# Optimization experiments

Measured on AMD Instinct MI355X. Metric: run time of the kernel, lower is better.

Reference implementation:

```python
import jax, jax.numpy as jnp
import numpy as np

THRESHOLD = 0.5
ALPHA = 1.0
N, D = 100000, 256
B, K = 1024, 128


def _l2norm(x):
    # F.normalize(x, p=2, dim=-1) with eps=1e-12
    return x / jnp.maximum(jnp.linalg.norm(x, axis=-1, keepdims=True), 1e-12)


def setup_inputs() -> dict:
    key = jax.random.key(0)
    k1, k2, k3, k4, k5, k6, k7 = jax.random.split(key, 7)
    feature = jax.random.normal(k1, (N, D), dtype=jnp.float32)
    text_embedding = jax.random.normal(k2, (N, D), dtype=jnp.float32)
    virtual = jax.random.normal(k3, (1, D), dtype=jnp.float32)
    # Gumbel(0,1) noise for gumbel_softmax (tau=1), materialized for determinism
    u = jax.random.uniform(k4, (B, K, K), dtype=jnp.float32, minval=1e-6, maxval=1.0 - 1e-6)
    gumbel = -jnp.log(-jnp.log(u))
    ego_nodes = jnp.sort(jax.random.randint(k5, (B, K), 0, N, dtype=jnp.int32), axis=-1)
    edges_adj = jax.random.randint(k6, (B, K, K), 0, 2, dtype=jnp.int32)
    train_label = jax.random.randint(k7, (B,), 0, 2, dtype=jnp.int32)
    return {"feature": feature, "text_embedding": text_embedding, "virtual": virtual,
            "gumbel": gumbel, "ego_nodes": ego_nodes, "edges_adj": edges_adj,
            "train_label": train_label}


def reference(feature, text_embedding, virtual, gumbel, ego_nodes, edges_adj, train_label):
    feat = _l2norm(feature)          # self.feature (normalized in __init__)
    emb = _l2norm(text_embedding)    # self.embedding
    te_local = _l2norm(emb - virtual)            # [N, D]

    tb = te_local[ego_nodes]                     # [B, K, D] gather per ego-subgraph
    sim = jnp.einsum('bkd,bjd->bkj', tb, tb) - THRESHOLD   # [B, K, K]
    sim_sub = jax.nn.softmax(sim + gumbel, axis=-1)         # gumbel_softmax, tau=1

    adj = edges_adj.astype(sim_sub.dtype)        # scatter edges_adj[src,dst]=1, precomputed
    # s_diff: row-wise L2 norm then mean over rows
    s_diff = jnp.sqrt(jnp.sum((adj - sim_sub) ** 2, axis=-1)).mean(axis=-1)   # [B]

    emb_out = feat[ego_nodes].mean(axis=1)       # [B, D] sum(feature)/n
    emb_pg = emb[ego_nodes].mean(axis=1)         # [B, D] sum(embedding)/n  (n == K)
    f_diff = jnp.linalg.norm(emb_out - emb_pg, axis=-1)                        # [B]

    score = s_diff + ALPHA * f_diff
    score = (score - score.min()) / (score.max() - score.min())

    y = train_label.astype(score.dtype)
    eps = 1e-7  # stabilizes log at exact 0/1 (torch BCELoss clamps log at -100)
    sc = jnp.clip(score, eps, 1.0 - eps)
    bce = -(y * jnp.log(sc) + (1.0 - y) * jnp.log1p(-sc)).mean()
    loss = bce / y.shape[0]
    return score, loss
```

## Files before the change

kernel.cpp:

```cpp
#include <hip/hip_runtime.h>
#include <math.h>

#define NROWS 100000
#define DIM 256
#define BB 1024
#define KK 128
#define PITCH 264

typedef __attribute__((ext_vector_type(8))) short short8;
typedef __attribute__((ext_vector_type(4))) float float4v;

__device__ __forceinline__ unsigned short f2bf(float x) {
    unsigned u = __float_as_uint(x);
    u += 0x7FFFu + ((u >> 16) & 1u);
    return (unsigned short)(u >> 16);
}

__global__ __launch_bounds__(512) void fused_main(
    const float* __restrict__ feature,
    const float* __restrict__ text,
    const float* __restrict__ virt,
    const float* __restrict__ gumbel,
    const int*   __restrict__ ego,
    const int*   __restrict__ adj,
    float*       __restrict__ score_raw)
{
    __shared__ unsigned short tb[KK * PITCH];
    __shared__ float fpart[8][DIM];
    __shared__ float spart[8];

    const int b    = blockIdx.x;
    const int tid  = threadIdx.x;
    const int wave = tid >> 6;
    const int lane = tid & 63;

    const float4 vv = ((const float4*)virt)[lane];

    float fa0 = 0.f, fa1 = 0.f, fa2 = 0.f, fa3 = 0.f;
    const int* ego_b = ego + b * KK;

    for (int k = wave * 16; k < wave * 16 + 16; ++k) {
        const int e = ego_b[k];
        const float4 t4 = ((const float4*)(text    + (size_t)e * DIM))[lane];
        const float4 f4 = ((const float4*)(feature + (size_t)e * DIM))[lane];

        float st = t4.x*t4.x + t4.y*t4.y + t4.z*t4.z + t4.w*t4.w;
        float sf = f4.x*f4.x + f4.y*f4.y + f4.z*f4.z + f4.w*f4.w;
        #pragma unroll
        for (int m = 1; m < 64; m <<= 1) {
            st += __shfl_xor(st, m);
            sf += __shfl_xor(sf, m);
        }
        const float inv_ne = 1.f / fmaxf(sqrtf(st), 1e-12f);
        const float inv_nf = 1.f / fmaxf(sqrtf(sf), 1e-12f);

        const float ex = t4.x * inv_ne, ey = t4.y * inv_ne;
        const float ez = t4.z * inv_ne, ew = t4.w * inv_ne;
        const float wx = ex - vv.x, wy = ey - vv.y;
        const float wz = ez - vv.z, ww = ew - vv.w;
        float sw = wx*wx + wy*wy + wz*wz + ww*ww;
        #pragma unroll
        for (int m = 1; m < 64; m <<= 1) sw += __shfl_xor(sw, m);
        const float inv_nt = 1.f / fmaxf(sqrtf(sw), 1e-12f);

        fa0 += f4.x * inv_nf - ex;
        fa1 += f4.y * inv_nf - ey;
        fa2 += f4.z * inv_nf - ez;
        fa3 += f4.w * inv_nf - ew;

        ushort4 pk;
        pk.x = f2bf(wx * inv_nt);
        pk.y = f2bf(wy * inv_nt);
        pk.z = f2bf(wz * inv_nt);
        pk.w = f2bf(ww * inv_nt);
        *(ushort4*)&tb[k * PITCH + 4 * lane] = pk;
    }
    fpart[wave][4*lane + 0] = fa0;
    fpart[wave][4*lane + 1] = fa1;
    fpart[wave][4*lane + 2] = fa2;
    fpart[wave][4*lane + 3] = fa3;
    __syncthreads();

    float4v acc[8];
    const float4v zero = {0.f, 0.f, 0.f, 0.f};
    #pragma unroll
    for (int t = 0; t < 8; ++t) acc[t] = zero;

    const int g = lane >> 4;
    const int c = lane & 15;

    #pragma unroll
    for (int q = 0; q < 8; ++q) {
        const int dq = q * 32 + g * 8;
        const short8 af = *(const short8*)&tb[(wave * 16 + c) * PITCH + dq];
        short8 bf0 = *(const short8*)&tb[(0*16 + c) * PITCH + dq];
        short8 bf1 = *(const short8*)&tb[(1*16 + c) * PITCH + dq];
        short8 bf2 = *(const short8*)&tb[(2*16 + c) * PITCH + dq];
        short8 bf3 = *(const short8*)&tb[(3*16 + c) * PITCH + dq];
        short8 bf4 = *(const short8*)&tb[(4*16 + c) * PITCH + dq];
        short8 bf5 = *(const short8*)&tb[(5*16 + c) * PITCH + dq];
        short8 bf6 = *(const short8*)&tb[(6*16 + c) * PITCH + dq];
        short8 bf7 = *(const short8*)&tb[(7*16 + c) * PITCH + dq];
        acc[0] = __builtin_amdgcn_mfma_f32_16x16x32_bf16(af, bf0, acc[0], 0, 0, 0);
        acc[1] = __builtin_amdgcn_mfma_f32_16x16x32_bf16(af, bf1, acc[1], 0, 0, 0);
        acc[2] = __builtin_amdgcn_mfma_f32_16x16x32_bf16(af, bf2, acc[2], 0, 0, 0);
        acc[3] = __builtin_amdgcn_mfma_f32_16x16x32_bf16(af, bf3, acc[3], 0, 0, 0);
        acc[4] = __builtin_amdgcn_mfma_f32_16x16x32_bf16(af, bf4, acc[4], 0, 0, 0);
        acc[5] = __builtin_amdgcn_mfma_f32_16x16x32_bf16(af, bf5, acc[5], 0, 0, 0);
        acc[6] = __builtin_amdgcn_mfma_f32_16x16x32_bf16(af, bf6, acc[6], 0, 0, 0);
        acc[7] = __builtin_amdgcn_mfma_f32_16x16x32_bf16(af, bf7, acc[7], 0, 0, 0);
    }

    const float* gb = gumbel + (size_t)b * KK * KK;
    const int*   ab = adj    + (size_t)b * KK * KK;
    float rs = 0.f;
    #pragma unroll
    for (int r = 0; r < 4; ++r) {
        const int krow = wave * 16 + g * 4 + r;
        const float* gr = gb + krow * KK + c;
        const int*   ar = ab + krow * KK + c;
        float v[8];
        float mx = -1e30f;
        #pragma unroll
        for (int t = 0; t < 8; ++t) {
            v[t] = acc[t][r] - 0.5f + gr[t * 16];
            mx = fmaxf(mx, v[t]);
        }
        #pragma unroll
        for (int msk = 1; msk < 16; msk <<= 1) mx = fmaxf(mx, __shfl_xor(mx, msk));
        float S = 0.f;
        #pragma unroll
        for (int t = 0; t < 8; ++t) { v[t] = __expf(v[t] - mx); S += v[t]; }
        #pragma unroll
        for (int msk = 1; msk < 16; msk <<= 1) S += __shfl_xor(S, msk);
        const float invS = 1.f / S;
        float T = 0.f;
        #pragma unroll
        for (int t = 0; t < 8; ++t) {
            const float d = (float)ar[t * 16] - v[t] * invS;
            T += d * d;
        }
        #pragma unroll
        for (int msk = 1; msk < 16; msk <<= 1) T += __shfl_xor(T, msk);
        rs += sqrtf(T);
    }
    rs += __shfl_xor(rs, 16);
    rs += __shfl_xor(rs, 32);
    if (lane == 0) spart[wave] = rs;
    __syncthreads();

    if (wave == 0) {
        float d0 = 0.f, d1 = 0.f, d2 = 0.f, d3 = 0.f;
        #pragma unroll
        for (int w = 0; w < 8; ++w) {
            d0 += fpart[w][lane];
            d1 += fpart[w][lane + 64];
            d2 += fpart[w][lane + 128];
            d3 += fpart[w][lane + 192];
        }
        const float inv = 1.f / 128.f;
        d0 *= inv; d1 *= inv; d2 *= inv; d3 *= inv;
        float q2 = d0*d0 + d1*d1 + d2*d2 + d3*d3;
        #pragma unroll
        for (int m = 1; m < 64; m <<= 1) q2 += __shfl_xor(q2, m);
        if (lane == 0) {
            float stot = 0.f;
            #pragma unroll
            for (int w = 0; w < 8; ++w) stot += spart[w];
            score_raw[b] = stot * (1.f / 128.f) + sqrtf(q2);
        }
    }
}

__global__ __launch_bounds__(1024) void finalize(
    const float* __restrict__ score_raw,
    const int*   __restrict__ label,
    float*       __restrict__ out)
{
    __shared__ float wmin[16], wmax[16], wsum[16];
    const int tid = threadIdx.x;
    const float s = score_raw[tid];
    float mn = s, mx = s;
    #pragma unroll
    for (int m = 1; m < 64; m <<= 1) {
        mn = fminf(mn, __shfl_xor(mn, m));
        mx = fmaxf(mx, __shfl_xor(mx, m));
    }
    if ((tid & 63) == 0) { wmin[tid >> 6] = mn; wmax[tid >> 6] = mx; }
    __syncthreads();
    float gmn = wmin[0], gmx = wmax[0];
    #pragma unroll
    for (int w = 1; w < 16; ++w) {
        gmn = fminf(gmn, wmin[w]);
        gmx = fmaxf(gmx, wmax[w]);
    }
    const float score = (s - gmn) / (gmx - gmn);
    out[tid] = score;

    const float y  = (float)label[tid];
    const float sc = fminf(fmaxf(score, 1e-7f), 1.f - 1e-7f);
    float term = -(y * logf(sc) + (1.f - y) * log1pf(-sc));
    #pragma unroll
    for (int m = 1; m < 64; m <<= 1) term += __shfl_xor(term, m);
    if ((tid & 63) == 0) wsum[tid >> 6] = term;
    __syncthreads();
    if (tid == 0) {
        float tot = 0.f;
        #pragma unroll
        for (int w = 0; w < 16; ++w) tot += wsum[w];
        out[BB] = tot / (1024.f * 1024.f);
    }
}

extern "C" void kernel_launch(void* const* d_in, const int* in_sizes, int n_in,
                              void* d_out, int out_size, void* d_ws, size_t ws_size,
                              hipStream_t stream) {
    const float* feature = (const float*)d_in[0];
    const float* text    = (const float*)d_in[1];
    const float* virt    = (const float*)d_in[2];
    const float* gumbel  = (const float*)d_in[3];
    const int*   ego     = (const int*)d_in[4];
    const int*   adj     = (const int*)d_in[5];
    const int*   label   = (const int*)d_in[6];
    float* out       = (float*)d_out;
    float* score_raw = (float*)d_ws;

    fused_main<<<BB, 512, 0, stream>>>(feature, text, virt, gumbel, ego, adj, score_raw);
    finalize<<<1, 1024, 0, stream>>>(score_raw, label, out);
}
```

Before: 82.86 us.

## Prefetch gathers, hoist gumbel/adj loads, algebraic softmax-diff without max pass

Gathered text and feature rows are double-buffered two at a time so the next rows load while the current ones are normalized. The norm of emb−virtual is derived algebraically from the dot with virtual, which removes a third cross-lane reduction. Gumbel and adjacency tiles are loaded with nontemporal loads before and around the MFMA loop to overlap their latency. The s_diff row norm is expanded into sums of exp, adj, and adj·exp without a max subtraction, which risks exp overflow and adds register pressure under a tighter launch bound.

```diff
diff --git a/kernel.cpp b/kernel.cpp
--- a/kernel.cpp
+++ b/kernel.cpp
@@ -1,7 +1,6 @@
 #include <hip/hip_runtime.h>
 #include <math.h>
 
-#define NROWS 100000
 #define DIM 256
 #define BB 1024
 #define KK 128
@@ -16,7 +15,11 @@
     return (unsigned short)(u >> 16);
 }
 
-__global__ __launch_bounds__(512) void fused_main(
+__device__ __forceinline__ float dot4(const float4 a, const float4 b) {
+    return a.x*b.x + a.y*b.y + a.z*b.z + a.w*b.w;
+}
+
+__global__ __launch_bounds__(512, 4) void fused_main(
     const float* __restrict__ feature,
     const float* __restrict__ text,
     const float* __restrict__ virt,
@@ -25,7 +28,7 @@
     const int*   __restrict__ adj,
     float*       __restrict__ score_raw)
 {
-    __shared__ unsigned short tb[KK * PITCH];
+    __shared__ unsigned short tbs[KK * PITCH];
     __shared__ float fpart[8][DIM];
     __shared__ float spart[8];
 
@@ -35,114 +38,139 @@
     const int lane = tid & 63;
 
     const float4 vv = ((const float4*)virt)[lane];
-
-    float fa0 = 0.f, fa1 = 0.f, fa2 = 0.f, fa3 = 0.f;
+    float vv2 = dot4(vv, vv);
+    #pragma unroll
+    for (int m = 1; m < 64; m <<= 1) vv2 += __shfl_xor(vv2, m);
+
     const int* ego_b = ego + b * KK;
-
-    for (int k = wave * 16; k < wave * 16 + 16; ++k) {
-        const int e = ego_b[k];
-        const float4 t4 = ((const float4*)(text    + (size_t)e * DIM))[lane];
-        const float4 f4 = ((const float4*)(feature + (size_t)e * DIM))[lane];
-
-        float st = t4.x*t4.x + t4.y*t4.y + t4.z*t4.z + t4.w*t4.w;
-        float sf = f4.x*f4.x + f4.y*f4.y + f4.z*f4.z + f4.w*f4.w;
+    const int  base  = wave * 16;
+
+    float fd0 = 0.f, fd1 = 0.f, fd2 = 0.f, fd3 = 0.f;
+
+    int ea = ego_b[base + 0], eb = ego_b[base + 1];
+    float4 nta = ((const float4*)(text    + (size_t)ea * DIM))[lane];
+    float4 nfa = ((const float4*)(feature + (size_t)ea * DIM))[lane];
+    float4 ntb = ((const float4*)(text    + (size_t)eb * DIM))[lane];
+    float4 nfb = ((const float4*)(feature + (size_t)eb * DIM))[lane];
+
+    #pragma unroll
+    for (int kk = 0; kk < 16; kk += 2) {
+        const float4 at = nta, af = nfa, bt = ntb, bf = nfb;
+        if (kk + 2 < 16) {
+            const int na = ego_b[base + kk + 2], nb = ego_b[base + kk + 3];
+            nta = ((const float4*)(text    + (size_t)na * DIM))[lane];
+            nfa = ((const float4*)(feature + (size_t)na * DIM))[lane];
+            ntb = ((const float4*)(text    + (size_t)nb * DIM))[lane];
+            nfb = ((const float4*)(feature + (size_t)nb * DIM))[lane];
+        }
+        float sta = dot4(at, at), sfa = dot4(af, af), sva = dot4(at, vv);
+        float stb = dot4(bt, bt), sfb = dot4(bf, bf), svb = dot4(bt, vv);
         #pragma unroll
         for (int m = 1; m < 64; m <<= 1) {
-            st += __shfl_xor(st, m);
-            sf += __shfl_xor(sf, m);
-        }
-        const float inv_ne = 1.f / fmaxf(sqrtf(st), 1e-12f);
-        const float inv_nf = 1.f / fmaxf(sqrtf(sf), 1e-12f);
-
-        const float ex = t4.x * inv_ne, ey = t4.y * inv_ne;
-        const float ez = t4.z * inv_ne, ew = t4.w * inv_ne;
-        const float wx = ex - vv.x, wy = ey - vv.y;
-        const float wz = ez - vv.z, ww = ew - vv.w;
-        float sw = wx*wx + wy*wy + wz*wz + ww*ww;
-        #pragma unroll
-        for (int m = 1; m < 64; m <<= 1) sw += __shfl_xor(sw, m);
-        const float inv_nt = 1.f / fmaxf(sqrtf(sw), 1e-12f);
-
-        fa0 += f4.x * inv_nf - ex;
-        fa1 += f4.y * inv_nf - ey;
-        fa2 += f4.z * inv_nf - ez;
-        fa3 += f4.w * inv_nf - ew;
-
-        ushort4 pk;
-        pk.x = f2bf(wx * inv_nt);
-        pk.y = f2bf(wy * inv_nt);
-        pk.z = f2bf(wz * inv_nt);
-        pk.w = f2bf(ww * inv_nt);
-        *(ushort4*)&tb[k * PITCH + 4 * lane] = pk;
-    }
-    fpart[wave][4*lane + 0] = fa0;
-    fpart[wave][4*lane + 1] = fa1;
-    fpart[wave][4*lane + 2] = fa2;
-    fpart[wave][4*lane + 3] = fa3;
-    __syncthreads();
+            sta += __shfl_xor(sta, m);  sfa += __shfl_xor(sfa, m);  sva += __shfl_xor(sva, m);
+            stb += __shfl_xor(stb, m);  sfb += __shfl_xor(sfb, m);  svb += __shfl_xor(svb, m);
+        }
+        {
+            const float inv_ne = 1.f / fmaxf(sqrtf(sta), 1e-12f);
+            const float inv_nf = 1.f / fmaxf(sqrtf(sfa), 1e-12f);
+            const float nw2    = fmaxf(1.f + vv2 - 2.f * sva * inv_ne, 0.f);
+            const float inv_nt = 1.f / fmaxf(sqrtf(nw2), 1e-12f);
+            const float ex = at.x*inv_ne, ey = at.y*inv_ne, ez = at.z*inv_ne, ew = at.w*inv_ne;
+            fd0 += af.x*inv_nf - ex;  fd1 += af.y*inv_nf - ey;
+            fd2 += af.z*inv_nf - ez;  fd3 += af.w*inv_nf - ew;
+            ushort4 pk;
+            pk.x = f2bf((ex - vv.x) * inv_nt);
+            pk.y = f2bf((ey - vv.y) * inv_nt);
+            pk.z = f2bf((ez - vv.z) * inv_nt);
+            pk.w = f2bf((ew - vv.w) * inv_nt);
+            *(ushort4*)&tbs[(base + kk) * PITCH + 4 * lane] = pk;
+        }
+        {
+            const float inv_ne = 1.f / fmaxf(sqrtf(stb), 1e-12f);
+            const float inv_nf = 1.f / fmaxf(sqrtf(sfb), 1e-12f);
+            const float nw2    = fmaxf(1.f + vv2 - 2.f * svb * inv_ne, 0.f);
+            const float inv_nt = 1.f / fmaxf(sqrtf(nw2), 1e-12f);
+            const float ex = bt.x*inv_ne, ey = bt.y*inv_ne, ez = bt.z*inv_ne, ew = bt.w*inv_ne;
+            fd0 += bf.x*inv_nf - ex;  fd1 += bf.y*inv_nf - ey;
+            fd2 += bf.z*inv_nf - ez;  fd3 += bf.w*inv_nf - ew;
+            ushort4 pk;
+            pk.x = f2bf((ex - vv.x) * inv_nt);
+            pk.y = f2bf((ey - vv.y) * inv_nt);
+            pk.z = f2bf((ez - vv.z) * inv_nt);
+            pk.w = f2bf((ew - vv.w) * inv_nt);
+            *(ushort4*)&tbs[(base + kk + 1) * PITCH + 4 * lane] = pk;
+        }
+    }
+    fpart[wave][4*lane + 0] = fd0;
+    fpart[wave][4*lane + 1] = fd1;
+    fpart[wave][4*lane + 2] = fd2;
+    fpart[wave][4*lane + 3] = fd3;
+    __syncthreads();
+
+    const int g = lane >> 4;
+    const int c = lane & 15;
+
+    const float* gb = gumbel + (size_t)b * KK * KK;
+    const int*   ab = adj    + (size_t)b * KK * KK;
+
+    float gvv[32];
+    #pragma unroll
+    for (int r = 0; r < 4; ++r) {
+        const float* gr = gb + (base + g*4 + r) * KK + c;
+        #pragma unroll
+        for (int t = 0; t < 8; ++t)
+            gvv[r*8 + t] = __builtin_nontemporal_load(gr + t*16);
+    }
 
     float4v acc[8];
     const float4v zero = {0.f, 0.f, 0.f, 0.f};
     #pragma unroll
     for (int t = 0; t < 8; ++t) acc[t] = zero;
 
-    const int g = lane >> 4;
-    const int c = lane & 15;
-
     #pragma unroll
     for (int q = 0; q < 8; ++q) {
         const int dq = q * 32 + g * 8;
-        const short8 af = *(const short8*)&tb[(wave * 16 + c) * PITCH + dq];
-        short8 bf0 = *(const short8*)&tb[(0*16 + c) * PITCH + dq];
-        short8 bf1 = *(const short8*)&tb[(1*16 + c) * PITCH + dq];
-        short8 bf2 = *(const short8*)&tb[(2*16 + c) * PITCH + dq];
-        short8 bf3 = *(const short8*)&tb[(3*16 + c) * PITCH + dq];
-        short8 bf4 = *(const short8*)&tb[(4*16 + c) * PITCH + dq];
-        short8 bf5 = *(const short8*)&tb[(5*16 + c) * PITCH + dq];
-        short8 bf6 = *(const short8*)&tb[(6*16 + c) * PITCH + dq];
-        short8 bf7 = *(const short8*)&tb[(7*16 + c) * PITCH + dq];
-        acc[0] = __builtin_amdgcn_mfma_f32_16x16x32_bf16(af, bf0, acc[0], 0, 0, 0);
-        acc[1] = __builtin_amdgcn_mfma_f32_16x16x32_bf16(af, bf1, acc[1], 0, 0, 0);
-        acc[2] = __builtin_amdgcn_mfma_f32_16x16x32_bf16(af, bf2, acc[2], 0, 0, 0);
-        acc[3] = __builtin_amdgcn_mfma_f32_16x16x32_bf16(af, bf3, acc[3], 0, 0, 0);
-        acc[4] = __builtin_amdgcn_mfma_f32_16x16x32_bf16(af, bf4, acc[4], 0, 0, 0);
-        acc[5] = __builtin_amdgcn_mfma_f32_16x16x32_bf16(af, bf5, acc[5], 0, 0, 0);
-        acc[6] = __builtin_amdgcn_mfma_f32_16x16x32_bf16(af, bf6, acc[6], 0, 0, 0);
-        acc[7] = __builtin_amdgcn_mfma_f32_16x16x32_bf16(af, bf7, acc[7], 0, 0, 0);
-    }
-
-    const float* gb = gumbel + (size_t)b * KK * KK;
-    const int*   ab = adj    + (size_t)b * KK * KK;
+        const short8 afr = *(const short8*)&tbs[(base + c) * PITCH + dq];
+        #pragma unroll
+        for (int t = 0; t < 8; ++t) {
+            const short8 bfr = *(const short8*)&tbs[(t*16 + c) * PITCH + dq];
+            acc[t] = __builtin_amdgcn_mfma_f32_16x16x32_bf16(afr, bfr, acc[t], 0, 0, 0);
+        }
+    }
+
+    int avv[32];
+    #pragma unroll
+    for (int r = 0; r < 4; ++r) {
+        const int* ar = ab + (base + g*4 + r) * KK + c;
+        #pragma unroll
+        for (int t = 0; t < 8; ++t)
+            avv[r*8 + t] = __builtin_nontemporal_load(ar + t*16);
+    }
+
     float rs = 0.f;
     #pragma unroll
     for (int r = 0; r < 4; ++r) {
-        const int krow = wave * 16 + g * 4 + r;
-        const float* gr = gb + krow * KK + c;
-        const int*   ar = ab + krow * KK + c;
-        float v[8];
-        float mx = -1e30f;
+        float s = 0.f, a1 = 0.f, a2 = 0.f, a3 = 0.f;
         #pragma unroll
         for (int t = 0; t < 8; ++t) {
-            v[t] = acc[t][r] - 0.5f + gr[t * 16];
-            mx = fmaxf(mx, v[t]);
-        }
-        #pragma unroll
-        for (int msk = 1; msk < 16; msk <<= 1) mx = fmaxf(mx, __shfl_xor(mx, msk));
-        float S = 0.f;
-        #pragma unroll
-        for (int t = 0; t < 8; ++t) { v[t] = __expf(v[t] - mx); S += v[t]; }
-        #pragma unroll
-        for (int msk = 1; msk < 16; msk <<= 1) S += __shfl_xor(S, msk);
-        const float invS = 1.f / S;
-        float T = 0.f;
-        #pragma unroll
-        for (int t = 0; t < 8; ++t) {
-            const float d = (float)ar[t * 16] - v[t] * invS;
-            T += d * d;
-        }
-        #pragma unroll
-        for (int msk = 1; msk < 16; msk <<= 1) T += __shfl_xor(T, msk);
-        rs += sqrtf(T);
+            const float vt = acc[t][r] - 0.5f + gvv[r*8 + t];
+            const float et = __expf(vt);
+            const float ad = (float)avv[r*8 + t];
+            s  += et;
+            a3 += et * et;
+            a1 += ad;
+            a2 += ad * et;
+        }
+        #pragma unroll
+        for (int msk = 1; msk < 16; msk <<= 1) {
+            s  += __shfl_xor(s,  msk);
+            a1 += __shfl_xor(a1, msk);
+            a2 += __shfl_xor(a2, msk);
+            a3 += __shfl_xor(a3, msk);
+        }
+        const float invS = 1.f / s;
+        const float T = a1 - 2.f * invS * a2 + invS * invS * a3;
+        rs += sqrtf(fmaxf(T, 0.f));
     }
     rs += __shfl_xor(rs, 16);
     rs += __shfl_xor(rs, 32);
```

Result: faster. 76.09 us (-8.2%).
